# Performance work log

Hardware: AMD Instinct MI355X
Metric: run time of the kernel (lower is better)

The kernel has to match this reference:

```python
import jax, jax.numpy as jnp
import numpy as np
import math

N, T, D = 4, 2048, 1024

def setup_inputs() -> dict:
    key = jax.random.key(0)
    ks = jax.random.split(key, 14)
    s = 1.0 / math.sqrt(D)
    p = {
        'X':  jax.random.normal(ks[0], (N, T, D), jnp.float32),
        'Wq': jax.random.uniform(ks[1], (D, D), jnp.float32, -s, s),
        'bq': jax.random.uniform(ks[2], (D,), jnp.float32, -s, s),
        'Wk': jax.random.uniform(ks[3], (D, D), jnp.float32, -s, s),
        'bk': jax.random.uniform(ks[4], (D,), jnp.float32, -s, s),
        'Wv': jax.random.uniform(ks[5], (D, D), jnp.float32, -s, s),
        'bv': jax.random.uniform(ks[6], (D,), jnp.float32, -s, s),
        'W1': jax.random.uniform(ks[7], (D, D), jnp.float32, -s, s),
        'b1': jax.random.uniform(ks[8], (D,), jnp.float32, -s, s),
        'W2': jax.random.uniform(ks[9], (D, D), jnp.float32, -s, s),
        'b2': jax.random.uniform(ks[10], (D,), jnp.float32, -s, s),
        'W3': jax.random.uniform(ks[11], (D, D), jnp.float32, -s, s),
        'b3': jax.random.uniform(ks[12], (D,), jnp.float32, -s, s),
        'g1': jnp.ones((D,), jnp.float32),  'be1': jnp.zeros((D,), jnp.float32),
        'g2': jnp.ones((D,), jnp.float32),  'be2': jnp.zeros((D,), jnp.float32),
    }
    return p

def _layer_norm(x, g, b, eps=1e-5):
    mu = jnp.mean(x, axis=-1, keepdims=True)
    var = jnp.mean(jnp.square(x - mu), axis=-1, keepdims=True)
    return (x - mu) * jax.lax.rsqrt(var + eps) * g + b

def reference(X, Wq, bq, Wk, bk, Wv, bv, W1, b1, W2, b2, W3, b3, g1, be1, g2, be2):
    d = X.shape[-1]
    q = X @ Wq + bq                      # (N,T,Dq)
    k = X @ Wk + bk
    v = X @ Wv + bv
    scores = jnp.einsum('ntd,nsd->nts', q, k) / jnp.sqrt(jnp.asarray(d, X.dtype))
    attn = jax.nn.softmax(scores, axis=-1)   # full (N,T,T), as in source
    ctx = jnp.einsum('nts,nsd->ntd', attn, v)
    h = _layer_norm(ctx + X, g1, be1)
    m = jax.nn.relu(h @ W1 + b1)
    m = jax.nn.relu(m @ W2 + b2)
    m = m @ W3 + b3
    return _layer_norm(m + h, g2, be2)
```

## Files before the change

kernel.cpp:

```cpp
#include <hip/hip_runtime.h>
#include <hip/hip_bf16.h>


typedef __attribute__((ext_vector_type(8))) short short8;
typedef __attribute__((ext_vector_type(4))) short short4v;
typedef __attribute__((ext_vector_type(4))) float float4v;

#define DEVI static __device__ __forceinline__

DEVI float bf2f(short s) {
  union { unsigned u; float f; } c;
  c.u = ((unsigned)(unsigned short)s) << 16;
  return c.f;
}
DEVI short f2bf(float f) {
  union { __hip_bfloat16 h; short s; } c;
  c.h = __float2bfloat16(f);
  return c.s;
}
DEVI void gload_lds16(const void* g, void* l) {
  __builtin_amdgcn_global_load_lds(
      (const __attribute__((address_space(1))) void*)g,
      (__attribute__((address_space(3))) void*)l, 16, 0, 0);
}

#define MFMA16 __builtin_amdgcn_mfma_f32_16x16x32_bf16
#define CFENCE asm volatile("" ::: "memory")
#define SCHEDB __builtin_amdgcn_sched_barrier(0)

__global__ __launch_bounds__(512, 4) void gemmTB(
    const short* __restrict__ A, const short* __restrict__ B,
    const float* __restrict__ bias, float alpha, void* __restrict__ Cout,
    int K, int lda, int ldb, int ldc,
    long sA, long sB, long sC, int flags)
{
  __shared__ __attribute__((aligned(16))) short lds[36864];

  const int tid  = threadIdx.x;
  const int lane = tid & 63;
  const int wid  = tid >> 6;
  const int wm = wid >> 1, wn = wid & 1;
  const int lr = lane & 15;
  const int kq = lane >> 4;

  const long m0 = (long)blockIdx.x * 256;
  const long n0 = (long)blockIdx.y * 128;
  const short* Ab = A + (long)blockIdx.z * sA;
  const short* Bb = B + (long)blockIdx.z * sB;

  const int sc8 = (((tid & 3) ^ ((tid >> 2) & 3)) << 3);
  const short* pA0 = Ab + (m0 + (tid >> 2)) * (long)lda + sc8;
  const short* pA1 = Ab + (m0 + 128 + (tid >> 2)) * (long)lda + sc8;
  const short* pB  = Bb + (n0 + (tid >> 2)) * (long)ldb + sc8;

  char* ldsB = (char*)lds;
  const int dst0 = tid * 16;

  auto stage = [&](int bs, int kt) {
    const long ko = (long)kt * 32;
    gload_lds16(pA0 + ko, ldsB + bs + dst0);
    gload_lds16(pA1 + ko, ldsB + bs + 8192 + dst0);
    gload_lds16(pB  + ko, ldsB + bs + 16384 + dst0);
  };

  const int swz = ((kq ^ (lr & 3)) << 4);
  const int baseA = (wm * 64 + lr) * 64 + swz;
  const int baseB = 16384 + (wn * 64 + lr) * 64 + swz;

  float4v acc[4][4];
#pragma unroll
  for (int m = 0; m < 4; ++m)
#pragma unroll
    for (int n = 0; n < 4; ++n)
#pragma unroll
      for (int i = 0; i < 4; ++i) acc[m][n][i] = 0.f;

  const int NT = K >> 5;

  stage(0, 0);
  stage(24576, 1);
  asm volatile("s_waitcnt vmcnt(3)" ::: "memory");
  __builtin_amdgcn_s_barrier();
  CFENCE;

  int bsR = 0;
  int bsS = 2 * 24576;

  for (int t = 0; t < NT; ++t) {
    if (t + 2 < NT) stage(bsS, t + 2);

    const char* rA = ldsB + (bsR + baseA);
    const char* rB = ldsB + (bsR + baseB);
    short8 a0 = *(const short8*)(rA);
    short8 a1 = *(const short8*)(rA + 1024);
    short8 a2 = *(const short8*)(rA + 2048);
    short8 a3 = *(const short8*)(rA + 3072);
    short8 b0 = *(const short8*)(rB);
    short8 b1 = *(const short8*)(rB + 1024);
    short8 b2 = *(const short8*)(rB + 2048);
    short8 b3 = *(const short8*)(rB + 3072);

    asm volatile("s_waitcnt lgkmcnt(0)" ::: "memory");
    SCHEDB;
    __builtin_amdgcn_s_setprio(1);
    acc[0][0] = MFMA16(a0, b0, acc[0][0], 0, 0, 0);
    acc[0][1] = MFMA16(a0, b1, acc[0][1], 0, 0, 0);
    acc[0][2] = MFMA16(a0, b2, acc[0][2], 0, 0, 0);
    acc[0][3] = MFMA16(a0, b3, acc[0][3], 0, 0, 0);
    acc[1][0] = MFMA16(a1, b0, acc[1][0], 0, 0, 0);
    acc[1][1] = MFMA16(a1, b1, acc[1][1], 0, 0, 0);
    acc[1][2] = MFMA16(a1, b2, acc[1][2], 0, 0, 0);
    acc[1][3] = MFMA16(a1, b3, acc[1][3], 0, 0, 0);
    acc[2][0] = MFMA16(a2, b0, acc[2][0], 0, 0, 0);
    acc[2][1] = MFMA16(a2, b1, acc[2][1], 0, 0, 0);
    acc[2][2] = MFMA16(a2, b2, acc[2][2], 0, 0, 0);
    acc[2][3] = MFMA16(a2, b3, acc[2][3], 0, 0, 0);
    acc[3][0] = MFMA16(a3, b0, acc[3][0], 0, 0, 0);
    acc[3][1] = MFMA16(a3, b1, acc[3][1], 0, 0, 0);
    acc[3][2] = MFMA16(a3, b2, acc[3][2], 0, 0, 0);
    acc[3][3] = MFMA16(a3, b3, acc[3][3], 0, 0, 0);
    __builtin_amdgcn_s_setprio(0);

    if (t + 2 < NT) { asm volatile("s_waitcnt vmcnt(3)" ::: "memory"); }
    else            { asm volatile("s_waitcnt vmcnt(0)" ::: "memory"); }
    __builtin_amdgcn_s_barrier();
    CFENCE;

    bsR = (bsR == 2 * 24576) ? 0 : bsR + 24576;
    bsS = (bsS == 2 * 24576) ? 0 : bsS + 24576;
  }

  const int dob = flags & 1, dor = flags & 2, f32o = flags & 4;
  float* Cf = (float*)Cout + (long)blockIdx.z * sC;
  short* Cb = (short*)Cout + (long)blockIdx.z * sC;
  const long r0 = m0 + wm * 64 + kq * 4;
  const long c0 = n0 + wn * 64 + lr;
#pragma unroll
  for (int m = 0; m < 4; ++m)
#pragma unroll
    for (int n = 0; n < 4; ++n) {
      const long c = c0 + n * 16;
      float bv = dob ? bias[c] : 0.f;
#pragma unroll
      for (int i = 0; i < 4; ++i) {
        const long r = r0 + m * 16 + i;
        float v = acc[m][n][i] * alpha + bv;
        if (dor) v = fmaxf(v, 0.f);
        if (f32o) Cf[r * ldc + c] = v;
        else      Cb[r * ldc + c] = f2bf(v);
      }
    }
}


__global__ __launch_bounds__(256) void cast_x_k(const float* __restrict__ X,
                                                short* __restrict__ Xb) {
  int i = blockIdx.x * 256 + threadIdx.x;
  float4v v = ((const float4v*)X)[i];
  short4v o;
#pragma unroll
  for (int j = 0; j < 4; ++j) o[j] = f2bf(v[j]);
  ((short4v*)Xb)[i] = o;
}

__global__ __launch_bounds__(256) void wcast_k(
    const float* __restrict__ Wq, const float* __restrict__ Wk,
    const float* __restrict__ Wv, const float* __restrict__ W1,
    const float* __restrict__ W2, const float* __restrict__ W3,
    const float* __restrict__ bq, const float* __restrict__ bk,
    const float* __restrict__ bv,
    short* __restrict__ Wqkvt, short* __restrict__ W1t,
    short* __restrict__ W2t, short* __restrict__ W3t,
    float* __restrict__ bqkv) {
  const int z = blockIdx.z;
  if (z == 6) {
    if (blockIdx.y != 0 || blockIdx.x >= 12) return;
    int i = blockIdx.x * 256 + threadIdx.x;
    bqkv[i] = i < 1024 ? bq[i] : (i < 2048 ? bk[i - 1024] : bv[i - 2048]);
    return;
  }
  const float* W = z == 0 ? Wq : z == 1 ? Wk : z == 2 ? Wv : z == 3 ? W1 : z == 4 ? W2 : W3;
  short* Wt = z == 0 ? Wqkvt : z == 1 ? Wqkvt + 1048576 : z == 2 ? Wqkvt + 2097152
            : z == 3 ? W1t : z == 4 ? W2t : W3t;
  __shared__ float tile[32][33];
  int tx = threadIdx.x & 31, ty = threadIdx.x >> 5;
  int c0 = blockIdx.x * 32, r0 = blockIdx.y * 32;
#pragma unroll
  for (int r = ty; r < 32; r += 8)
    tile[r][tx] = W[(long)(r0 + r) * 1024 + c0 + tx];
  __syncthreads();
#pragma unroll
  for (int r = ty; r < 32; r += 8)
    Wt[(long)(c0 + r) * 1024 + r0 + tx] = f2bf(tile[tx][r]);
}

__global__ __launch_bounds__(256) void tv_k(const short* __restrict__ qkv,
                                            short* __restrict__ vT) {
  __shared__ short tile[32][33];
  int b = blockIdx.z;
  int tx = threadIdx.x & 31, ty = threadIdx.x >> 5;
  int d0 = blockIdx.x * 32, t0 = blockIdx.y * 32;
#pragma unroll
  for (int r = ty; r < 32; r += 8)
    tile[r][tx] = qkv[((long)(b * 2048 + t0 + r)) * 3072 + 2048 + d0 + tx];
  __syncthreads();
#pragma unroll
  for (int r = ty; r < 32; r += 8)
    vT[(long)b * 2097152 + (long)(d0 + r) * 2048 + t0 + tx] = tile[tx][r];
}

__global__ __launch_bounds__(256) void softmax_k(short* __restrict__ s) {
  __shared__ float red[8];
  long r = blockIdx.x;
  short* p = s + r * 2048;
  int tid = threadIdx.x;
  short8 raw = *(short8*)&p[tid * 8];
  float v[8];
  float mx = -1e30f;
#pragma unroll
  for (int j = 0; j < 8; ++j) { v[j] = bf2f(raw[j]); mx = fmaxf(mx, v[j]); }
#pragma unroll
  for (int o = 32; o; o >>= 1) mx = fmaxf(mx, __shfl_xor(mx, o));
  if ((tid & 63) == 0) red[tid >> 6] = mx;
  __syncthreads();
  mx = fmaxf(fmaxf(red[0], red[1]), fmaxf(red[2], red[3]));
  float sum = 0.f;
#pragma unroll
  for (int j = 0; j < 8; ++j) { v[j] = __expf(v[j] - mx); sum += v[j]; }
#pragma unroll
  for (int o = 32; o; o >>= 1) sum += __shfl_xor(sum, o);
  if ((tid & 63) == 0) red[4 + (tid >> 6)] = sum;
  __syncthreads();
  float inv = 1.f / (red[4] + red[5] + red[6] + red[7]);
  short8 o8;
#pragma unroll
  for (int j = 0; j < 8; ++j) o8[j] = f2bf(v[j] * inv);
  *(short8*)&p[tid * 8] = o8;
}

__global__ __launch_bounds__(256) void addln_k(const float* __restrict__ a,
                                               const float* __restrict__ b,
                                               const float* __restrict__ g,
                                               const float* __restrict__ be,
                                               float* __restrict__ outf,
                                               short* __restrict__ outb) {
  __shared__ float red[8];
  long r = blockIdx.x;
  int tid = threadIdx.x;
  float4v va = ((const float4v*)(a + r * 1024))[tid];
  float4v vb = ((const float4v*)(b + r * 1024))[tid];
  float x[4]; float s = 0.f;
#pragma unroll
  for (int j = 0; j < 4; ++j) { x[j] = va[j] + vb[j]; s += x[j]; }
#pragma unroll
  for (int o = 32; o; o >>= 1) s += __shfl_xor(s, o);
  if ((tid & 63) == 0) red[tid >> 6] = s;
  __syncthreads();
  float mu = (red[0] + red[1] + red[2] + red[3]) * (1.f / 1024.f);
  float ss = 0.f;
#pragma unroll
  for (int j = 0; j < 4; ++j) { float d = x[j] - mu; ss += d * d; }
#pragma unroll
  for (int o = 32; o; o >>= 1) ss += __shfl_xor(ss, o);
  if ((tid & 63) == 0) red[4 + (tid >> 6)] = ss;
  __syncthreads();
  float var = (red[4] + red[5] + red[6] + red[7]) * (1.f / 1024.f);
  float rstd = rsqrtf(var + 1e-5f);
  float4v vg = ((const float4v*)g)[tid];
  float4v vbe = ((const float4v*)be)[tid];
  float4v y;
#pragma unroll
  for (int j = 0; j < 4; ++j) y[j] = (x[j] - mu) * rstd * vg[j] + vbe[j];
  ((float4v*)(outf + r * 1024))[tid] = y;
  if (outb) {
    short4v ob;
#pragma unroll
    for (int j = 0; j < 4; ++j) ob[j] = f2bf(y[j]);
    ((short4v*)(outb + r * 1024))[tid] = ob;
  }
}


extern "C" void kernel_launch(void* const* d_in, const int* in_sizes, int n_in,
                              void* d_out, int out_size, void* d_ws, size_t ws_size,
                              hipStream_t stream) {
  const float* X  = (const float*)d_in[0];
  const float* Wq = (const float*)d_in[1];
  const float* bq = (const float*)d_in[2];
  const float* Wk = (const float*)d_in[3];
  const float* bk = (const float*)d_in[4];
  const float* Wv = (const float*)d_in[5];
  const float* bv = (const float*)d_in[6];
  const float* W1 = (const float*)d_in[7];
  const float* b1 = (const float*)d_in[8];
  const float* W2 = (const float*)d_in[9];
  const float* b2 = (const float*)d_in[10];
  const float* W3 = (const float*)d_in[11];
  const float* b3 = (const float*)d_in[12];
  const float* g1  = (const float*)d_in[13];
  const float* be1 = (const float*)d_in[14];
  const float* g2  = (const float*)d_in[15];
  const float* be2 = (const float*)d_in[16];

  char* ws = (char*)d_ws;
  short* Xb     = (short*)(ws + 0);
  short* Wqkvt  = (short*)(ws + 16777216);
  short* W1t    = (short*)(ws + 23068672);
  short* W2t    = (short*)(ws + 25165824);
  short* W3t    = (short*)(ws + 27262976);
  float* bqkv   = (float*)(ws + 29360128);
  short* qkv    = (short*)(ws + 29372416);
  short* vT     = (short*)(ws + 79704064);
  short* scores = (short*)(ws + 96481280);
  float* ctx    = (float*)(ws + 29372416);
  float* h      = (float*)(ws + 96481280);
  short* hb     = (short*)(ws + 0);
  short* m1     = (short*)(ws + 29372416);
  short* m2     = (short*)(ws + 46149632);
  float* m3     = (float*)(ws + 62926848);
  float* out    = (float*)d_out;

  cast_x_k<<<8192, 256, 0, stream>>>(X, Xb);
  wcast_k<<<dim3(32, 32, 7), 256, 0, stream>>>(Wq, Wk, Wv, W1, W2, W3,
                                               bq, bk, bv,
                                               Wqkvt, W1t, W2t, W3t, bqkv);

  gemmTB<<<dim3(32, 24, 1), 512, 0, stream>>>(
      Xb, Wqkvt, bqkv, 1.0f, qkv, 1024, 1024, 1024, 3072, 0, 0, 0, 1);

  tv_k<<<dim3(32, 64, 4), 256, 0, stream>>>(qkv, vT);

  gemmTB<<<dim3(8, 16, 4), 512, 0, stream>>>(
      qkv, qkv + 1024, nullptr, 0.03125f, scores, 1024, 3072, 3072, 2048,
      (long)2048 * 3072, (long)2048 * 3072, (long)2048 * 2048, 0);

  softmax_k<<<8192, 256, 0, stream>>>(scores);

  gemmTB<<<dim3(8, 8, 4), 512, 0, stream>>>(
      scores, vT, nullptr, 1.0f, ctx, 2048, 2048, 2048, 1024,
      (long)2048 * 2048, (long)1024 * 2048, (long)2048 * 1024, 4);

  addln_k<<<8192, 256, 0, stream>>>(ctx, X, g1, be1, h, hb);

  gemmTB<<<dim3(32, 8, 1), 512, 0, stream>>>(
      hb, W1t, b1, 1.0f, m1, 1024, 1024, 1024, 1024, 0, 0, 0, 3);
  gemmTB<<<dim3(32, 8, 1), 512, 0, stream>>>(
      m1, W2t, b2, 1.0f, m2, 1024, 1024, 1024, 1024, 0, 0, 0, 3);
  gemmTB<<<dim3(32, 8, 1), 512, 0, stream>>>(
      m2, W3t, b3, 1.0f, m3, 1024, 1024, 1024, 1024, 0, 0, 0, 5);

  addln_k<<<8192, 256, 0, stream>>>(m3, h, g2, be2, out, nullptr);
}
```

Before: 309.8 us.

## Restructure GEMM into 128x128 tiles with 4-stage LDS ring and fragment prefetch

The GEMM kernel changes from 512-thread blocks with 256x128 tiles and a 3-stage LDS ring to 256-thread blocks with 128x128 tiles and a 4-stage ring. The main loop is unrolled by two, and the LDS fragments for the next k-step are read while the current MFMAs run, so LDS latency overlaps with compute. The swizzle patterns are changed to fit the new layout. Smaller tiles double the grid size, which should fill the CUs better, but each block reuses less data and uses more registers for the double fragment buffers.

```diff
diff --git a/kernel.cpp b/kernel.cpp
--- a/kernel.cpp
+++ b/kernel.cpp
@@ -28,13 +28,13 @@
 #define CFENCE asm volatile("" ::: "memory")
 #define SCHEDB __builtin_amdgcn_sched_barrier(0)
 
-__global__ __launch_bounds__(512, 4) void gemmTB(
+__global__ __launch_bounds__(256, 2) void gemmP(
     const short* __restrict__ A, const short* __restrict__ B,
     const float* __restrict__ bias, float alpha, void* __restrict__ Cout,
     int K, int lda, int ldb, int ldc,
     long sA, long sB, long sC, int flags)
 {
-  __shared__ __attribute__((aligned(16))) short lds[36864];
+  __shared__ __attribute__((aligned(16))) short lds[32768];
 
   const int tid  = threadIdx.x;
   const int lane = tid & 63;
@@ -43,15 +43,16 @@
   const int lr = lane & 15;
   const int kq = lane >> 4;
 
-  const long m0 = (long)blockIdx.x * 256;
+  const long m0 = (long)blockIdx.x * 128;
   const long n0 = (long)blockIdx.y * 128;
   const short* Ab = A + (long)blockIdx.z * sA;
   const short* Bb = B + (long)blockIdx.z * sB;
 
-  const int sc8 = (((tid & 3) ^ ((tid >> 2) & 3)) << 3);
+  const int sc8 = (((tid & 3) ^ ((tid >> 3) & 3)) << 3);
   const short* pA0 = Ab + (m0 + (tid >> 2)) * (long)lda + sc8;
-  const short* pA1 = Ab + (m0 + 128 + (tid >> 2)) * (long)lda + sc8;
-  const short* pB  = Bb + (n0 + (tid >> 2)) * (long)ldb + sc8;
+  const short* pA1 = Ab + (m0 + 64 + (tid >> 2)) * (long)lda + sc8;
+  const short* pB0 = Bb + (n0 + (tid >> 2)) * (long)ldb + sc8;
+  const short* pB1 = Bb + (n0 + 64 + (tid >> 2)) * (long)ldb + sc8;
 
   char* ldsB = (char*)lds;
   const int dst0 = tid * 16;
@@ -59,13 +60,27 @@
   auto stage = [&](int bs, int kt) {
     const long ko = (long)kt * 32;
     gload_lds16(pA0 + ko, ldsB + bs + dst0);
-    gload_lds16(pA1 + ko, ldsB + bs + 8192 + dst0);
-    gload_lds16(pB  + ko, ldsB + bs + 16384 + dst0);
+    gload_lds16(pA1 + ko, ldsB + bs + 4096 + dst0);
+    gload_lds16(pB0 + ko, ldsB + bs + 8192 + dst0);
+    gload_lds16(pB1 + ko, ldsB + bs + 12288 + dst0);
   };
 
-  const int swz = ((kq ^ (lr & 3)) << 4);
+  const int swz = ((kq ^ ((lr >> 1) & 3)) << 4);
   const int baseA = (wm * 64 + lr) * 64 + swz;
-  const int baseB = 16384 + (wn * 64 + lr) * 64 + swz;
+  const int baseB = 8192 + (wn * 64 + lr) * 64 + swz;
+
+  auto rdfrags = [&](int bs, short8* a, short8* b) {
+    const char* rA = ldsB + bs + baseA;
+    const char* rB = ldsB + bs + baseB;
+    a[0] = *(const short8*)(rA);
+    a[1] = *(const short8*)(rA + 1024);
+    a[2] = *(const short8*)(rA + 2048);
+    a[3] = *(const short8*)(rA + 3072);
+    b[0] = *(const short8*)(rB);
+    b[1] = *(const short8*)(rB + 1024);
+    b[2] = *(const short8*)(rB + 2048);
+    b[3] = *(const short8*)(rB + 3072);
+  };
 
   float4v acc[4][4];
 #pragma unroll
@@ -75,59 +90,61 @@
 #pragma unroll
       for (int i = 0; i < 4; ++i) acc[m][n][i] = 0.f;
 
+  auto mfma16x = [&](short8* a, short8* b) {
+#pragma unroll
+    for (int m = 0; m < 4; ++m)
+#pragma unroll
+      for (int n = 0; n < 4; ++n)
+        acc[m][n] = MFMA16(a[m], b[n], acc[m][n], 0, 0, 0);
+  };
+
   const int NT = K >> 5;
 
-  stage(0, 0);
-  stage(24576, 1);
-  asm volatile("s_waitcnt vmcnt(3)" ::: "memory");
-  __builtin_amdgcn_s_barrier();
-  CFENCE;
-
-  int bsR = 0;
-  int bsS = 2 * 24576;
-
-  for (int t = 0; t < NT; ++t) {
-    if (t + 2 < NT) stage(bsS, t + 2);
-
-    const char* rA = ldsB + (bsR + baseA);
-    const char* rB = ldsB + (bsR + baseB);
-    short8 a0 = *(const short8*)(rA);
-    short8 a1 = *(const short8*)(rA + 1024);
-    short8 a2 = *(const short8*)(rA + 2048);
-    short8 a3 = *(const short8*)(rA + 3072);
-    short8 b0 = *(const short8*)(rB);
-    short8 b1 = *(const short8*)(rB + 1024);
-    short8 b2 = *(const short8*)(rB + 2048);
-    short8 b3 = *(const short8*)(rB + 3072);
-
-    asm volatile("s_waitcnt lgkmcnt(0)" ::: "memory");
+  int B0 = 0, B1 = 16384, B2 = 32768, B3 = 49152;
+
+  stage(B0, 0); stage(B1, 1); stage(B2, 2);
+  asm volatile("s_waitcnt vmcnt(8)" ::: "memory");
+  __builtin_amdgcn_s_barrier(); CFENCE;
+  short8 aP[4], bP[4], aQ[4], bQ[4];
+  rdfrags(B0, aP, bP);
+  asm volatile("s_waitcnt vmcnt(4)" ::: "memory");
+  __builtin_amdgcn_s_barrier(); CFENCE;
+
+  for (int t = 0; t < NT; t += 2) {
+    if (t + 3 < NT) {
+      stage(B3, t + 3);
+      asm volatile("s_waitcnt vmcnt(4)" ::: "memory");
+    } else if (t + 2 < NT) {
+      asm volatile("s_waitcnt vmcnt(0)" ::: "memory");
+    }
+    rdfrags(B1, aQ, bQ);
+    asm volatile("s_waitcnt lgkmcnt(8)" ::: "memory");
     SCHEDB;
     __builtin_amdgcn_s_setprio(1);
-    acc[0][0] = MFMA16(a0, b0, acc[0][0], 0, 0, 0);
-    acc[0][1] = MFMA16(a0, b1, acc[0][1], 0, 0, 0);
-    acc[0][2] = MFMA16(a0, b2, acc[0][2], 0, 0, 0);
-    acc[0][3] = MFMA16(a0, b3, acc[0][3], 0, 0, 0);
-    acc[1][0] = MFMA16(a1, b0, acc[1][0], 0, 0, 0);
-    acc[1][1] = MFMA16(a1, b1, acc[1][1], 0, 0, 0);
-    acc[1][2] = MFMA16(a1, b2, acc[1][2], 0, 0, 0);
-    acc[1][3] = MFMA16(a1, b3, acc[1][3], 0, 0, 0);
-    acc[2][0] = MFMA16(a2, b0, acc[2][0], 0, 0, 0);
-    acc[2][1] = MFMA16(a2, b1, acc[2][1], 0, 0, 0);
-    acc[2][2] = MFMA16(a2, b2, acc[2][2], 0, 0, 0);
-    acc[2][3] = MFMA16(a2, b3, acc[2][3], 0, 0, 0);
-    acc[3][0] = MFMA16(a3, b0, acc[3][0], 0, 0, 0);
-    acc[3][1] = MFMA16(a3, b1, acc[3][1], 0, 0, 0);
-    acc[3][2] = MFMA16(a3, b2, acc[3][2], 0, 0, 0);
-    acc[3][3] = MFMA16(a3, b3, acc[3][3], 0, 0, 0);
+    mfma16x(aP, bP);
     __builtin_amdgcn_s_setprio(0);
-
-    if (t + 2 < NT) { asm volatile("s_waitcnt vmcnt(3)" ::: "memory"); }
-    else            { asm volatile("s_waitcnt vmcnt(0)" ::: "memory"); }
-    __builtin_amdgcn_s_barrier();
-    CFENCE;
-
-    bsR = (bsR == 2 * 24576) ? 0 : bsR + 24576;
-    bsS = (bsS == 2 * 24576) ? 0 : bsS + 24576;
+    __builtin_amdgcn_s_barrier(); CFENCE;
+
+    if (t + 4 < NT) {
+      stage(B0, t + 4);
+      asm volatile("s_waitcnt vmcnt(4)" ::: "memory");
+    } else if (t + 3 < NT) {
+      asm volatile("s_waitcnt vmcnt(0)" ::: "memory");
+    }
+    if (t + 2 < NT) {
+      rdfrags(B2, aP, bP);
+      asm volatile("s_waitcnt lgkmcnt(8)" ::: "memory");
+    } else {
+      asm volatile("s_waitcnt lgkmcnt(0)" ::: "memory");
+    }
+    SCHEDB;
+    __builtin_amdgcn_s_setprio(1);
+    mfma16x(aQ, bQ);
+    __builtin_amdgcn_s_setprio(0);
+    __builtin_amdgcn_s_barrier(); CFENCE;
+
+    int tmp = B0; B0 = B2; B2 = tmp;
+    tmp = B1; B1 = B3; B3 = tmp;
   }
 
   const int dob = flags & 1, dor = flags & 2, f32o = flags & 4;
@@ -325,28 +342,28 @@
                                                bq, bk, bv,
                                                Wqkvt, W1t, W2t, W3t, bqkv);
 
-  gemmTB<<<dim3(32, 24, 1), 512, 0, stream>>>(
+  gemmP<<<dim3(64, 24, 1), 256, 0, stream>>>(
       Xb, Wqkvt, bqkv, 1.0f, qkv, 1024, 1024, 1024, 3072, 0, 0, 0, 1);
 
   tv_k<<<dim3(32, 64, 4), 256, 0, stream>>>(qkv, vT);
 
-  gemmTB<<<dim3(8, 16, 4), 512, 0, stream>>>(
+  gemmP<<<dim3(16, 16, 4), 256, 0, stream>>>(
       qkv, qkv + 1024, nullptr, 0.03125f, scores, 1024, 3072, 3072, 2048,
       (long)2048 * 3072, (long)2048 * 3072, (long)2048 * 2048, 0);
 
   softmax_k<<<8192, 256, 0, stream>>>(scores);
 
-  gemmTB<<<dim3(8, 8, 4), 512, 0, stream>>>(
+  gemmP<<<dim3(16, 8, 4), 256, 0, stream>>>(
       scores, vT, nullptr, 1.0f, ctx, 2048, 2048, 2048, 1024,
       (long)2048 * 2048, (long)1024 * 2048, (long)2048 * 1024, 4);
 
   addln_k<<<8192, 256, 0, stream>>>(ctx, X, g1, be1, h, hb);
 
-  gemmTB<<<dim3(32, 8, 1), 512, 0, stream>>>(
+  gemmP<<<dim3(64, 8, 1), 256, 0, stream>>>(
       hb, W1t, b1, 1.0f, m1, 1024, 1024, 1024, 1024, 0, 0, 0, 3);
-  gemmTB<<<dim3(32, 8, 1), 512, 0, stream>>>(
+  gemmP<<<dim3(64, 8, 1), 256, 0, stream>>>(
       m1, W2t, b2, 1.0f, m2, 1024, 1024, 1024, 1024, 0, 0, 0, 3);
-  gemmTB<<<dim3(32, 8, 1), 512, 0, stream>>>(
+  gemmP<<<dim3(64, 8, 1), 256, 0, stream>>>(
       m2, W3t, b3, 1.0f, m3, 1024, 1024, 1024, 1024, 0, 0, 0, 5);
 
   addln_k<<<8192, 256, 0, stream>>>(m3, h, g2, be2, out, nullptr);
```

After: 332.9 us. 7.5% more time.

## Template GEMM on N-tile width and pick per-GEMM tile sizes for better occupancy

Applied to the files above, without the earlier changes.

Turns the GEMM kernel into a template over the number of N fragments per wave, so the block N-tile becomes 64, 96 or 128 columns. The LDS buffer size, B-loader thread count, waitcnt values and accumulators scale with it. The QKV GEMM uses 96-wide tiles and the PV and MLP GEMMs use 64-wide tiles, which gives more blocks to fill the CUs. It also changes the LDS swizzle pattern. Narrower tiles lower arithmetic intensity and mean more redundant A loads.

```diff
diff --git a/kernel.cpp b/kernel.cpp
--- a/kernel.cpp
+++ b/kernel.cpp
@@ -28,13 +28,15 @@
 #define CFENCE asm volatile("" ::: "memory")
 #define SCHEDB __builtin_amdgcn_sched_barrier(0)
 
-__global__ __launch_bounds__(512, 4) void gemmTB(
+template <int NFB>
+__global__ __launch_bounds__(512, 4) void gemmT(
     const short* __restrict__ A, const short* __restrict__ B,
     const float* __restrict__ bias, float alpha, void* __restrict__ Cout,
     int K, int lda, int ldb, int ldc,
     long sA, long sB, long sC, int flags)
 {
-  __shared__ __attribute__((aligned(16))) short lds[36864];
+  constexpr int BUFB = 16384 + NFB * 2048;
+  __shared__ __attribute__((aligned(16))) char lds[3 * BUFB];
 
   const int tid  = threadIdx.x;
   const int lane = tid & 63;
@@ -44,47 +46,49 @@
   const int kq = lane >> 4;
 
   const long m0 = (long)blockIdx.x * 256;
-  const long n0 = (long)blockIdx.y * 128;
+  const long n0 = (long)blockIdx.y * (NFB * 32);
   const short* Ab = A + (long)blockIdx.z * sA;
   const short* Bb = B + (long)blockIdx.z * sB;
 
-  const int sc8 = (((tid & 3) ^ ((tid >> 2) & 3)) << 3);
+  const int sc8 = (((tid & 3) ^ ((tid >> 3) & 3)) << 3);
   const short* pA0 = Ab + (m0 + (tid >> 2)) * (long)lda + sc8;
   const short* pA1 = Ab + (m0 + 128 + (tid >> 2)) * (long)lda + sc8;
   const short* pB  = Bb + (n0 + (tid >> 2)) * (long)ldb + sc8;
 
-  char* ldsB = (char*)lds;
+  char* ldsB = lds;
   const int dst0 = tid * 16;
+  const bool bldr = tid < NFB * 128;
 
   auto stage = [&](int bs, int kt) {
     const long ko = (long)kt * 32;
     gload_lds16(pA0 + ko, ldsB + bs + dst0);
     gload_lds16(pA1 + ko, ldsB + bs + 8192 + dst0);
-    gload_lds16(pB  + ko, ldsB + bs + 16384 + dst0);
+    if (bldr) gload_lds16(pB + ko, ldsB + bs + 16384 + dst0);
   };
 
-  const int swz = ((kq ^ (lr & 3)) << 4);
+  const int swz = ((kq ^ ((lr >> 1) & 3)) << 4);
   const int baseA = (wm * 64 + lr) * 64 + swz;
-  const int baseB = 16384 + (wn * 64 + lr) * 64 + swz;
-
-  float4v acc[4][4];
+  const int baseB = 16384 + (wn * (NFB * 16) + lr) * 64 + swz;
+
+  float4v acc[4][NFB];
 #pragma unroll
   for (int m = 0; m < 4; ++m)
 #pragma unroll
-    for (int n = 0; n < 4; ++n)
+    for (int n = 0; n < NFB; ++n)
 #pragma unroll
       for (int i = 0; i < 4; ++i) acc[m][n][i] = 0.f;
 
   const int NT = K >> 5;
 
   stage(0, 0);
-  stage(24576, 1);
-  asm volatile("s_waitcnt vmcnt(3)" ::: "memory");
+  stage(BUFB, 1);
+  if (wid < 2 * NFB) { asm volatile("s_waitcnt vmcnt(3)" ::: "memory"); }
+  else               { asm volatile("s_waitcnt vmcnt(2)" ::: "memory"); }
   __builtin_amdgcn_s_barrier();
   CFENCE;
 
   int bsR = 0;
-  int bsS = 2 * 24576;
+  int bsS = 2 * BUFB;
 
   for (int t = 0; t < NT; ++t) {
     if (t + 2 < NT) stage(bsS, t + 2);
@@ -95,50 +99,44 @@
     short8 a1 = *(const short8*)(rA + 1024);
     short8 a2 = *(const short8*)(rA + 2048);
     short8 a3 = *(const short8*)(rA + 3072);
-    short8 b0 = *(const short8*)(rB);
-    short8 b1 = *(const short8*)(rB + 1024);
-    short8 b2 = *(const short8*)(rB + 2048);
-    short8 b3 = *(const short8*)(rB + 3072);
+    short8 bf[NFB];
+#pragma unroll
+    for (int n = 0; n < NFB; ++n) bf[n] = *(const short8*)(rB + n * 1024);
 
     asm volatile("s_waitcnt lgkmcnt(0)" ::: "memory");
     SCHEDB;
     __builtin_amdgcn_s_setprio(1);
-    acc[0][0] = MFMA16(a0, b0, acc[0][0], 0, 0, 0);
-    acc[0][1] = MFMA16(a0, b1, acc[0][1], 0, 0, 0);
-    acc[0][2] = MFMA16(a0, b2, acc[0][2], 0, 0, 0);
-    acc[0][3] = MFMA16(a0, b3, acc[0][3], 0, 0, 0);
-    acc[1][0] = MFMA16(a1, b0, acc[1][0], 0, 0, 0);
-    acc[1][1] = MFMA16(a1, b1, acc[1][1], 0, 0, 0);
-    acc[1][2] = MFMA16(a1, b2, acc[1][2], 0, 0, 0);
-    acc[1][3] = MFMA16(a1, b3, acc[1][3], 0, 0, 0);
-    acc[2][0] = MFMA16(a2, b0, acc[2][0], 0, 0, 0);
-    acc[2][1] = MFMA16(a2, b1, acc[2][1], 0, 0, 0);
-    acc[2][2] = MFMA16(a2, b2, acc[2][2], 0, 0, 0);
-    acc[2][3] = MFMA16(a2, b3, acc[2][3], 0, 0, 0);
-    acc[3][0] = MFMA16(a3, b0, acc[3][0], 0, 0, 0);
-    acc[3][1] = MFMA16(a3, b1, acc[3][1], 0, 0, 0);
-    acc[3][2] = MFMA16(a3, b2, acc[3][2], 0, 0, 0);
-    acc[3][3] = MFMA16(a3, b3, acc[3][3], 0, 0, 0);
+#pragma unroll
+    for (int n = 0; n < NFB; ++n) {
+      acc[0][n] = MFMA16(a0, bf[n], acc[0][n], 0, 0, 0);
+      acc[1][n] = MFMA16(a1, bf[n], acc[1][n], 0, 0, 0);
+      acc[2][n] = MFMA16(a2, bf[n], acc[2][n], 0, 0, 0);
+      acc[3][n] = MFMA16(a3, bf[n], acc[3][n], 0, 0, 0);
+    }
     __builtin_amdgcn_s_setprio(0);
 
-    if (t + 2 < NT) { asm volatile("s_waitcnt vmcnt(3)" ::: "memory"); }
-    else            { asm volatile("s_waitcnt vmcnt(0)" ::: "memory"); }
+    if (t + 2 < NT) {
+      if (wid < 2 * NFB) { asm volatile("s_waitcnt vmcnt(3)" ::: "memory"); }
+      else               { asm volatile("s_waitcnt vmcnt(2)" ::: "memory"); }
+    } else {
+      asm volatile("s_waitcnt vmcnt(0)" ::: "memory");
+    }
     __builtin_amdgcn_s_barrier();
     CFENCE;
 
-    bsR = (bsR == 2 * 24576) ? 0 : bsR + 24576;
-    bsS = (bsS == 2 * 24576) ? 0 : bsS + 24576;
+    bsR = (bsR == 2 * BUFB) ? 0 : bsR + BUFB;
+    bsS = (bsS == 2 * BUFB) ? 0 : bsS + BUFB;
   }
 
   const int dob = flags & 1, dor = flags & 2, f32o = flags & 4;
   float* Cf = (float*)Cout + (long)blockIdx.z * sC;
   short* Cb = (short*)Cout + (long)blockIdx.z * sC;
   const long r0 = m0 + wm * 64 + kq * 4;
-  const long c0 = n0 + wn * 64 + lr;
+  const long c0 = n0 + wn * (NFB * 16) + lr;
 #pragma unroll
   for (int m = 0; m < 4; ++m)
 #pragma unroll
-    for (int n = 0; n < 4; ++n) {
+    for (int n = 0; n < NFB; ++n) {
       const long c = c0 + n * 16;
       float bv = dob ? bias[c] : 0.f;
 #pragma unroll
@@ -325,28 +323,28 @@
                                                bq, bk, bv,
                                                Wqkvt, W1t, W2t, W3t, bqkv);
 
-  gemmTB<<<dim3(32, 24, 1), 512, 0, stream>>>(
+  gemmT<3><<<dim3(32, 32, 1), 512, 0, stream>>>(
       Xb, Wqkvt, bqkv, 1.0f, qkv, 1024, 1024, 1024, 3072, 0, 0, 0, 1);
 
   tv_k<<<dim3(32, 64, 4), 256, 0, stream>>>(qkv, vT);
 
-  gemmTB<<<dim3(8, 16, 4), 512, 0, stream>>>(
+  gemmT<4><<<dim3(8, 16, 4), 512, 0, stream>>>(
       qkv, qkv + 1024, nullptr, 0.03125f, scores, 1024, 3072, 3072, 2048,
       (long)2048 * 3072, (long)2048 * 3072, (long)2048 * 2048, 0);
 
   softmax_k<<<8192, 256, 0, stream>>>(scores);
 
-  gemmTB<<<dim3(8, 8, 4), 512, 0, stream>>>(
+  gemmT<2><<<dim3(8, 16, 4), 512, 0, stream>>>(
       scores, vT, nullptr, 1.0f, ctx, 2048, 2048, 2048, 1024,
       (long)2048 * 2048, (long)1024 * 2048, (long)2048 * 1024, 4);
 
   addln_k<<<8192, 256, 0, stream>>>(ctx, X, g1, be1, h, hb);
 
-  gemmTB<<<dim3(32, 8, 1), 512, 0, stream>>>(
+  gemmT<2><<<dim3(32, 16, 1), 512, 0, stream>>>(
       hb, W1t, b1, 1.0f, m1, 1024, 1024, 1024, 1024, 0, 0, 0, 3);
-  gemmTB<<<dim3(32, 8, 1), 512, 0, stream>>>(
+  gemmT<2><<<dim3(32, 16, 1), 512, 0, stream>>>(
       m1, W2t, b2, 1.0f, m2, 1024, 1024, 1024, 1024, 0, 0, 0, 3);
-  gemmTB<<<dim3(32, 8, 1), 512, 0, stream>>>(
+  gemmT<2><<<dim3(32, 16, 1), 512, 0, stream>>>(
       m2, W3t, b3, 1.0f, m3, 1024, 1024, 1024, 1024, 0, 0, 0, 5);
 
   addln_k<<<8192, 256, 0, stream>>>(m3, h, g2, be2, out, nullptr);
```

Measured after the change: 327.6 us. 1.06x slower.
